# Kernel optimization log

Hardware: AMD Instinct MI355X
Metric: run time of the kernel (lower is better)

## Reference

```python
import jax, jax.numpy as jnp
import numpy as np

N_NODES = 100_000
N_EDGES = 1_600_000
IN_DIM = 500
HID = 128
OUT = 16
DEG = 3          # Chebyshev 'order' -> DEG+1 basis terms
N_KAN_USED = 2   # forward applies kan_layers[:num_layers-1] with num_layers=3


def spmm(edge_index, h):
    # torch.sparse.mm(A, h) with A = COO(edge_index, ones, (N, N)):
    # out[row] = sum over edges of h[col]
    return jax.ops.segment_sum(h[edge_index[1]], edge_index[0], num_segments=N_NODES)


def cheb_kan(h, coeffs):
    # ChebyKANLayer: t = tanh(h); basis T_k(t) = cos(k*arccos(t)) computed via
    # the (mathematically identical, numerically stable) recurrence.
    t = jnp.tanh(h)                                  # [N, HID]
    Ts = [jnp.ones_like(t), t]
    for _ in range(DEG - 1):
        Ts.append(2.0 * t * Ts[-1] - Ts[-2])
    basis = jnp.stack(Ts, axis=-1)                   # [N, HID, DEG+1]
    return jnp.einsum('nid,iod->no', basis, coeffs)  # [N, HID]


def setup_inputs() -> dict:
    key = jax.random.key(0)
    ks = jax.random.split(key, 6)
    x = jax.random.normal(ks[0], (N_NODES, IN_DIM), dtype=jnp.float32)
    edge_index = jax.random.randint(ks[1], (2, N_EDGES), 0, N_NODES)
    W_in = jax.random.normal(ks[2], (IN_DIM, HID), dtype=jnp.float32) / np.sqrt(IN_DIM)
    cheb_coeffs = jax.random.normal(ks[3], (N_KAN_USED, HID, HID, DEG + 1),
                                    dtype=jnp.float32) / (HID * (DEG + 1))
    W_out = jax.random.normal(ks[4], (HID, OUT), dtype=jnp.float32) / np.sqrt(HID)
    return {"x": x, "edge_index": edge_index, "W_in": W_in,
            "cheb_coeffs": cheb_coeffs, "W_out": W_out}


def reference(x, edge_index, W_in, cheb_coeffs, W_out):
    h = x @ W_in                      # linear_input (no bias)
    # dropout is identity at inference
    h = spmm(edge_index, h)           # sparse adjacency aggregation
    for l in range(N_KAN_USED):
        h = cheb_kan(h, cheb_coeffs[l])
        h = spmm(edge_index, h)
    logits = h @ W_out                # output_layer (no bias)
    return jax.nn.log_softmax(logits, axis=-1)
```

## Files before the change

### kernel.cpp

```cpp
#include <hip/hip_runtime.h>
#include <hip/hip_bf16.h>

#define N_NODES 100000
#define N_EDGES 1600000
#define IN_DIM  500
#define HID     128
#define KDIM    512
#define NB      782
#define BCAP    4096

typedef __attribute__((ext_vector_type(8))) short bf16x8;
typedef __attribute__((ext_vector_type(4))) float f32x4;

__device__ inline short f2bf(float x) {
    union { float f; unsigned u; } v; v.f = x;
    unsigned r = (v.u + 0x7FFFu + ((v.u >> 16) & 1u)) >> 16;
    return (short)r;
}
__device__ inline float bf_lo(unsigned u) { union { unsigned u; float f; } v; v.u = u << 16; return v.f; }
__device__ inline float bf_hi(unsigned u) { union { unsigned u; float f; } v; v.u = u & 0xFFFF0000u; return v.f; }
__device__ inline float bf2f(unsigned short s) { union { unsigned u; float f; } v; v.u = ((unsigned)s) << 16; return v.f; }


__global__ __launch_bounds__(256) void bin_kernel(const int* __restrict__ ei,
                                                  int* __restrict__ bcnt,
                                                  unsigned* __restrict__ buf) {
    int e = blockIdx.x * 256 + threadIdx.x;
    if (e < N_EDGES) {
        int r = ei[e];
        int c = ei[N_EDGES + e];
        int b = r >> 7;
        int p = atomicAdd(&bcnt[b * 16], 1);
        if (p < BCAP) buf[b * BCAP + p] = ((unsigned)(r & 127) << 17) | (unsigned)c;
    }
}

__global__ __launch_bounds__(1024) void bscan_kernel(const int* __restrict__ bcnt,
                                                     int* __restrict__ bbase) {
    __shared__ int buf[1024];
    const int tid = threadIdx.x;
    int v = (tid < NB) ? bcnt[tid * 16] : 0;
    buf[tid] = v;
    __syncthreads();
    for (int off = 1; off < 1024; off <<= 1) {
        int t = (tid >= off) ? buf[tid - off] : 0;
        __syncthreads();
        buf[tid] += t;
        __syncthreads();
    }
    if (tid < NB) bbase[tid] = buf[tid] - v;
}

__global__ __launch_bounds__(256) void place_kernel(const unsigned* __restrict__ buf,
                                                    const int* __restrict__ bcnt,
                                                    const int* __restrict__ bbase,
                                                    int* __restrict__ row_start,
                                                    int* __restrict__ col_sorted) {
    __shared__ int hist[128];
    __shared__ int scan[128];
    __shared__ int cur[128];
    const int b = blockIdx.x, tid = threadIdx.x;
    int cnt = bcnt[b * 16]; if (cnt > BCAP) cnt = BCAP;
    const int base = bbase[b];
    if (tid < 128) hist[tid] = 0;
    __syncthreads();
    for (int i = tid; i < cnt; i += 256)
        atomicAdd(&hist[buf[b * BCAP + i] >> 17], 1);
    __syncthreads();
    if (tid < 128) scan[tid] = hist[tid];
    __syncthreads();
    for (int off = 1; off < 128; off <<= 1) {
        int t = (tid < 128 && tid >= off) ? scan[tid - off] : 0;
        __syncthreads();
        if (tid < 128) scan[tid] += t;
        __syncthreads();
    }
    if (tid < 128) {
        int excl = scan[tid] - hist[tid] + base;
        cur[tid] = excl;
        int r = b * 128 + tid;
        if (r < N_NODES) row_start[r] = excl;
        if (r == N_NODES - 1) row_start[N_NODES] = excl + hist[tid];
    }
    __syncthreads();
    for (int i = tid; i < cnt; i += 256) {
        unsigned u = buf[b * BCAP + i];
        int rl = (int)(u >> 17);
        int c  = (int)(u & 0x1FFFFu);
        int pos = atomicAdd(&cur[rl], 1);
        col_sorted[pos] = c;
    }
}

__global__ __launch_bounds__(256) void repack_cheb(const float* __restrict__ cheb,
                                                   unsigned short* __restrict__ Bmat) {
    int idx = blockIdx.x * 256 + threadIdx.x;
    int o = idx >> 9;
    int k = idx & 511;
    int i = k >> 2;
    int d = k & 3;
    Bmat[idx] = (unsigned short)f2bf(cheb[i * 512 + o * 4 + d]);
}
__global__ __launch_bounds__(256) void repack_w(const float* __restrict__ W,
                                                unsigned short* __restrict__ Wmat) {
    int idx = blockIdx.x * 256 + threadIdx.x;
    int o = idx >> 9;
    int k = idx & 511;
    Wmat[idx] = (k < IN_DIM) ? (unsigned short)f2bf(W[k * HID + o]) : 0;
}
__global__ __launch_bounds__(256) void repack_c2w(const float* __restrict__ cheb,
                                                  const float* __restrict__ Wout,
                                                  unsigned short* __restrict__ C2W) {
    int idx = blockIdx.x * 256 + threadIdx.x;
    if (idx >= 16 * 512) return;
    int o16 = idx >> 9;
    int k   = idx & 511;
    const float* cb = cheb + 65536 + (k >> 2) * 512 + (k & 3);
    float s = 0.f;
#pragma unroll 4
    for (int o = 0; o < 128; o++) s += cb[o * 4] * Wout[o * 16 + o16];
    C2W[o16 * 512 + k] = (unsigned short)f2bf(s);
}

__global__ __launch_bounds__(256, 4) void gemm_xw(const float* __restrict__ x,
                                                  const unsigned short* __restrict__ Wmat,
                                                  unsigned short* __restrict__ out) {
    __shared__ __align__(16) short As[2][64][40];
    __shared__ __align__(16) short Bs[2][128][40];
    const int tid  = threadIdx.x;
    const int lane = tid & 63;
    const int wave = tid >> 6;
    const int quad = lane >> 4;
    const int l16  = lane & 15;
    const int n0   = blockIdx.x * 64;
    const int ar   = tid >> 2;
    const int ah   = tid & 3;
    const int br   = tid >> 1;
    const int bh   = tid & 1;

    int nA = n0 + ar; if (nA >= N_NODES) nA = N_NODES - 1;
    const float* __restrict__ xrow = x + (long)nA * IN_DIM;

    f32x4 acc[8];
#pragma unroll
    for (int nt = 0; nt < 8; nt++)
#pragma unroll
        for (int r = 0; r < 4; r++) acc[nt][r] = 0.f;

    auto loadA = [&](int kt, float (&v)[8]) {
        const int kb = kt * 32 + ah * 8;
        if (kb + 8 <= IN_DIM) {
            const float4* s4 = (const float4*)(xrow + kb);
            float4 a0 = s4[0], a1 = s4[1];
            v[0]=a0.x; v[1]=a0.y; v[2]=a0.z; v[3]=a0.w;
            v[4]=a1.x; v[5]=a1.y; v[6]=a1.z; v[7]=a1.w;
        } else {
#pragma unroll
            for (int q = 0; q < 8; q++) v[q] = (kb + q < IN_DIM) ? xrow[kb + q] : 0.f;
        }
    };
    auto loadB = [&](int kt, bf16x8 (&w)[2]) {
        w[0] = *(const bf16x8*)&Wmat[br * 512 + kt * 32 + bh * 16];
        w[1] = *(const bf16x8*)&Wmat[br * 512 + kt * 32 + bh * 16 + 8];
    };
    auto storeA = [&](int buf, const float (&v)[8]) {
        short t[8];
#pragma unroll
        for (int q = 0; q < 8; q++) t[q] = f2bf(v[q]);
        *(bf16x8*)&As[buf][ar][ah * 8] = *(bf16x8*)&t[0];
    };
    auto storeB = [&](int buf, const bf16x8 (&w)[2]) {
        *(bf16x8*)&Bs[buf][br][bh * 16]     = w[0];
        *(bf16x8*)&Bs[buf][br][bh * 16 + 8] = w[1];
    };
    auto mfmaTile = [&](int buf) {
        bf16x8 a = *(const bf16x8*)&As[buf][wave * 16 + l16][quad * 8];
#pragma unroll
        for (int nt = 0; nt < 8; nt++) {
            bf16x8 b = *(const bf16x8*)&Bs[buf][nt * 16 + l16][quad * 8];
            acc[nt] = __builtin_amdgcn_mfma_f32_16x16x32_bf16(a, b, acc[nt], 0, 0, 0);
        }
    };

    float  va[8], vb[8];
    bf16x8 wa[2], wb[2];
    loadA(0, va); loadB(0, wa);
    for (int kt = 0; kt < 16; kt += 2) {
        storeA(0, va); storeB(0, wa);
        loadA(kt + 1, vb); loadB(kt + 1, wb);
        __syncthreads();
        mfmaTile(0);
        storeA(1, vb); storeB(1, wb);
        if (kt + 2 < 16) { loadA(kt + 2, va); loadB(kt + 2, wa); }
        __syncthreads();
        mfmaTile(1);
    }

    {
        int mrow = n0 + wave * 16 + quad * 4;
#pragma unroll
        for (int r = 0; r < 4; r++) {
            int n = mrow + r;
            if (n < N_NODES) {
#pragma unroll
                for (int nt = 0; nt < 8; nt++)
                    out[(long)n * HID + nt * 16 + l16] = (unsigned short)f2bf(acc[nt][r]);
            }
        }
    }
}

__global__ __launch_bounds__(256, 4) void cheb_gemm(const unsigned short* __restrict__ h,
                                                    const unsigned short* __restrict__ Bmat,
                                                    unsigned short* __restrict__ out) {
    __shared__ __align__(16) short As[2][64][40];
    __shared__ __align__(16) short Bs[2][128][40];
    const int tid  = threadIdx.x;
    const int lane = tid & 63;
    const int wave = tid >> 6;
    const int quad = lane >> 4;
    const int l16  = lane & 15;
    const int n0   = blockIdx.x * 64;
    const int ar   = tid >> 2;
    const int sub  = tid & 3;
    const int br   = tid >> 1;
    const int bh   = tid & 1;

    int nA = n0 + ar; if (nA >= N_NODES) nA = N_NODES - 1;
    const unsigned short* __restrict__ hrow = h + (long)nA * HID;

    f32x4 acc[8];
#pragma unroll
    for (int nt = 0; nt < 8; nt++)
#pragma unroll
        for (int r = 0; r < 4; r++) acc[nt][r] = 0.f;

    auto loadA = [&](int kt, unsigned& v) {
        v = *(const unsigned*)(hrow + kt * 8 + sub * 2);
    };
    auto loadB = [&](int kt, bf16x8 (&w)[2]) {
        w[0] = *(const bf16x8*)&Bmat[br * 512 + kt * 32 + bh * 16];
        w[1] = *(const bf16x8*)&Bmat[br * 512 + kt * 32 + bh * 16 + 8];
    };
    auto storeA = [&](int buf, unsigned v) {
        float hx[2] = {bf_lo(v), bf_hi(v)};
        short t[8];
#pragma unroll
        for (int q = 0; q < 2; q++) {
            float xx = fminf(fmaxf(hx[q], -15.f), 15.f);
            float e  = __expf(2.f * xx);
            float tt = (e - 1.f) / (e + 1.f);
            float T2 = 2.f * tt * tt - 1.f;
            float T3 = 2.f * tt * T2 - tt;
            t[q * 4 + 0] = (short)0x3F80;
            t[q * 4 + 1] = f2bf(tt);
            t[q * 4 + 2] = f2bf(T2);
            t[q * 4 + 3] = f2bf(T3);
        }
        *(bf16x8*)&As[buf][ar][sub * 8] = *(bf16x8*)&t[0];
    };
    auto storeB = [&](int buf, const bf16x8 (&w)[2]) {
        *(bf16x8*)&Bs[buf][br][bh * 16]     = w[0];
        *(bf16x8*)&Bs[buf][br][bh * 16 + 8] = w[1];
    };
    auto mfmaTile = [&](int buf) {
        bf16x8 a = *(const bf16x8*)&As[buf][wave * 16 + l16][quad * 8];
#pragma unroll
        for (int nt = 0; nt < 8; nt++) {
            bf16x8 b = *(const bf16x8*)&Bs[buf][nt * 16 + l16][quad * 8];
            acc[nt] = __builtin_amdgcn_mfma_f32_16x16x32_bf16(a, b, acc[nt], 0, 0, 0);
        }
    };

    unsigned va, vb;
    bf16x8   wa[2], wb[2];
    loadA(0, va); loadB(0, wa);
    for (int kt = 0; kt < 16; kt += 2) {
        storeA(0, va); storeB(0, wa);
        loadA(kt + 1, vb); loadB(kt + 1, wb);
        __syncthreads();
        mfmaTile(0);
        storeA(1, vb); storeB(1, wb);
        if (kt + 2 < 16) { loadA(kt + 2, va); loadB(kt + 2, wa); }
        __syncthreads();
        mfmaTile(1);
    }

    {
        int mrow = n0 + wave * 16 + quad * 4;
#pragma unroll
        for (int r = 0; r < 4; r++) {
            int n = mrow + r;
            if (n < N_NODES) {
#pragma unroll
                for (int nt = 0; nt < 8; nt++)
                    out[(long)n * HID + nt * 16 + l16] = (unsigned short)f2bf(acc[nt][r]);
            }
        }
    }
}

__global__ __launch_bounds__(256, 4) void cheb16_gemm(const unsigned short* __restrict__ h,
                                                      const unsigned short* __restrict__ C2W,
                                                      float* __restrict__ z) {
    __shared__ __align__(16) short As[2][64][40];
    __shared__ __align__(16) short Bs16[16][520];
    const int tid  = threadIdx.x;
    const int lane = tid & 63;
    const int wave = tid >> 6;
    const int quad = lane >> 4;
    const int l16  = lane & 15;
    const int n0   = blockIdx.x * 64;
    const int ar   = tid >> 2;
    const int sub  = tid & 3;

    {
        int o16 = tid >> 4;
        int seg = tid & 15;
        *(bf16x8*)&Bs16[o16][seg * 32]      = *(const bf16x8*)&C2W[o16 * 512 + seg * 32];
        *(bf16x8*)&Bs16[o16][seg * 32 + 8]  = *(const bf16x8*)&C2W[o16 * 512 + seg * 32 + 8];
        *(bf16x8*)&Bs16[o16][seg * 32 + 16] = *(const bf16x8*)&C2W[o16 * 512 + seg * 32 + 16];
        *(bf16x8*)&Bs16[o16][seg * 32 + 24] = *(const bf16x8*)&C2W[o16 * 512 + seg * 32 + 24];
    }

    int nA = n0 + ar; if (nA >= N_NODES) nA = N_NODES - 1;
    const unsigned short* __restrict__ hrow = h + (long)nA * HID;

    f32x4 acc;
#pragma unroll
    for (int r = 0; r < 4; r++) acc[r] = 0.f;

    auto loadA = [&](int kt, unsigned& v) {
        v = *(const unsigned*)(hrow + kt * 8 + sub * 2);
    };
    auto storeA = [&](int buf, unsigned v) {
        float hx[2] = {bf_lo(v), bf_hi(v)};
        short t[8];
#pragma unroll
        for (int q = 0; q < 2; q++) {
            float xx = fminf(fmaxf(hx[q], -15.f), 15.f);
            float e  = __expf(2.f * xx);
            float tt = (e - 1.f) / (e + 1.f);
            float T2 = 2.f * tt * tt - 1.f;
            float T3 = 2.f * tt * T2 - tt;
            t[q * 4 + 0] = (short)0x3F80;
            t[q * 4 + 1] = f2bf(tt);
            t[q * 4 + 2] = f2bf(T2);
            t[q * 4 + 3] = f2bf(T3);
        }
        *(bf16x8*)&As[buf][ar][sub * 8] = *(bf16x8*)&t[0];
    };
    auto mfmaTile = [&](int buf, int kt) {
        bf16x8 a = *(const bf16x8*)&As[buf][wave * 16 + l16][quad * 8];
        bf16x8 b = *(const bf16x8*)&Bs16[l16][kt * 32 + quad * 8];
        acc = __builtin_amdgcn_mfma_f32_16x16x32_bf16(a, b, acc, 0, 0, 0);
    };

    unsigned va, vb;
    loadA(0, va);
    for (int kt = 0; kt < 16; kt += 2) {
        storeA(0, va);
        loadA(kt + 1, vb);
        __syncthreads();
        mfmaTile(0, kt);
        storeA(1, vb);
        if (kt + 2 < 16) loadA(kt + 2, va);
        __syncthreads();
        mfmaTile(1, kt + 1);
    }

    {
        int mrow = n0 + wave * 16 + quad * 4;
#pragma unroll
        for (int r = 0; r < 4; r++) {
            int n = mrow + r;
            if (n < N_NODES) z[n * 16 + l16] = acc[r];
        }
    }
}

__global__ __launch_bounds__(256) void spmm_gather(const int* __restrict__ row_start,
                                                   const int* __restrict__ col_sorted,
                                                   const unsigned short* __restrict__ h,
                                                   unsigned short* __restrict__ out) {
    const int wid  = (blockIdx.x * 256 + threadIdx.x) >> 6;
    const int lane = threadIdx.x & 63;
    const int sub  = lane >> 4;
    const int fl   = lane & 15;
    if (wid >= N_NODES) return;
    const int s = row_start[wid];
    const int e = row_start[wid + 1];
    const uint4* __restrict__ h4 = (const uint4*)h;

    float a[8], b[8];
#pragma unroll
    for (int q = 0; q < 8; q++) { a[q] = 0.f; b[q] = 0.f; }

    int j = s;
    for (; j + 8 <= e; j += 8) {
        int c0 = col_sorted[j + sub];
        int c1 = col_sorted[j + 4 + sub];
        uint4 u0 = h4[c0 * 16 + fl];
        uint4 u1 = h4[c1 * 16 + fl];
        a[0] += bf_lo(u0.x); a[1] += bf_hi(u0.x);
        a[2] += bf_lo(u0.y); a[3] += bf_hi(u0.y);
        a[4] += bf_lo(u0.z); a[5] += bf_hi(u0.z);
        a[6] += bf_lo(u0.w); a[7] += bf_hi(u0.w);
        b[0] += bf_lo(u1.x); b[1] += bf_hi(u1.x);
        b[2] += bf_lo(u1.y); b[3] += bf_hi(u1.y);
        b[4] += bf_lo(u1.z); b[5] += bf_hi(u1.z);
        b[6] += bf_lo(u1.w); b[7] += bf_hi(u1.w);
    }
    for (; j < e; j += 4) {
        int idx = j + sub;
        float m = (idx < e) ? 1.f : 0.f;
        int ci = (idx < e) ? idx : (e - 1);
        int c = col_sorted[ci];
        uint4 u = h4[c * 16 + fl];
        a[0] = fmaf(m, bf_lo(u.x), a[0]); a[1] = fmaf(m, bf_hi(u.x), a[1]);
        a[2] = fmaf(m, bf_lo(u.y), a[2]); a[3] = fmaf(m, bf_hi(u.y), a[3]);
        a[4] = fmaf(m, bf_lo(u.z), a[4]); a[5] = fmaf(m, bf_hi(u.z), a[5]);
        a[6] = fmaf(m, bf_lo(u.w), a[6]); a[7] = fmaf(m, bf_hi(u.w), a[7]);
    }
#pragma unroll
    for (int q = 0; q < 8; q++) a[q] += b[q];
#pragma unroll
    for (int q = 0; q < 8; q++) {
        a[q] += __shfl_xor(a[q], 16);
        a[q] += __shfl_xor(a[q], 32);
    }
    if (sub == 0) {
        unsigned w0 = (unsigned)(unsigned short)f2bf(a[0]) | ((unsigned)(unsigned short)f2bf(a[1]) << 16);
        unsigned w1 = (unsigned)(unsigned short)f2bf(a[2]) | ((unsigned)(unsigned short)f2bf(a[3]) << 16);
        unsigned w2 = (unsigned)(unsigned short)f2bf(a[4]) | ((unsigned)(unsigned short)f2bf(a[5]) << 16);
        unsigned w3 = (unsigned)(unsigned short)f2bf(a[6]) | ((unsigned)(unsigned short)f2bf(a[7]) << 16);
        uint4 pw; pw.x = w0; pw.y = w1; pw.z = w2; pw.w = w3;
        ((uint4*)out)[wid * 16 + fl] = pw;
    }
}

__global__ __launch_bounds__(256) void spmm_out(const int* __restrict__ row_start,
                                                const int* __restrict__ col_sorted,
                                                const float* __restrict__ z,
                                                float* __restrict__ out) {
    const int wid  = (blockIdx.x * 256 + threadIdx.x) >> 6;
    const int lane = threadIdx.x & 63;
    const int sub  = lane >> 4;
    const int fl   = lane & 15;
    if (wid >= N_NODES) return;
    const int s = row_start[wid];
    const int e = row_start[wid + 1];

    float a0 = 0.f, a1 = 0.f;
    int j = s;
    for (; j + 8 <= e; j += 8) {
        int c0 = col_sorted[j + sub];
        int c1 = col_sorted[j + 4 + sub];
        a0 += z[c0 * 16 + fl];
        a1 += z[c1 * 16 + fl];
    }
    for (; j < e; j += 4) {
        int idx = j + sub;
        float m = (idx < e) ? 1.f : 0.f;
        int ci = (idx < e) ? idx : (e - 1);
        a0 = fmaf(m, z[col_sorted[ci] * 16 + fl], a0);
    }
    float v = a0 + a1;
    v += __shfl_xor(v, 16);
    v += __shfl_xor(v, 32);
    float mx = v;
#pragma unroll
    for (int m = 8; m >= 1; m >>= 1) mx = fmaxf(mx, __shfl_xor(mx, m));
    float ex = expf(v - mx);
    float se = ex;
#pragma unroll
    for (int m = 8; m >= 1; m >>= 1) se += __shfl_xor(se, m);
    if (sub == 0) out[wid * 16 + fl] = v - mx - logf(se);
}


extern "C" void kernel_launch(void* const* d_in, const int* in_sizes, int n_in,
                              void* d_out, int out_size, void* d_ws, size_t ws_size,
                              hipStream_t stream) {
    const float* x     = (const float*)d_in[0];
    const int*   ei    = (const int*)d_in[1];
    const float* W_in  = (const float*)d_in[2];
    const float* cheb  = (const float*)d_in[3];
    const float* W_out = (const float*)d_in[4];
    float* out = (float*)d_out;

    char* p = (char*)d_ws;
    unsigned short* hA   = (unsigned short*)p; p += (size_t)N_NODES * HID * 2;
    unsigned short* hB   = (unsigned short*)p; p += (size_t)N_NODES * HID * 2;
    int*   col_sorted    = (int*)p;            p += (size_t)N_EDGES * 4;
    unsigned short* Bmat = (unsigned short*)p; p += (size_t)HID * KDIM * 2;
    unsigned short* Wmat = (unsigned short*)p; p += (size_t)HID * KDIM * 2;
    unsigned short* C2W  = (unsigned short*)p; p += (size_t)16 * KDIM * 2;
    float* zbuf          = (float*)p;          p += (size_t)N_NODES * 16 * 4;
    int*   row_start     = (int*)p;            p += (size_t)(N_NODES + 1) * 4;
    int*   bcnt          = (int*)p;            p += (size_t)NB * 16 * 4;
    int*   bbase         = (int*)p;            p += (size_t)NB * 4;

    unsigned* bbuf = (unsigned*)hA;

    const int nblk_gemm = (N_NODES + 63) / 64;
    const int nblk_edge = N_EDGES / 256;
    const int nblk_spmm = (N_NODES + 3) / 4;

    hipMemsetAsync(bcnt, 0, (size_t)NB * 16 * 4, stream);
    bin_kernel<<<nblk_edge, 256, 0, stream>>>(ei, bcnt, bbuf);
    bscan_kernel<<<1, 1024, 0, stream>>>(bcnt, bbase);
    place_kernel<<<NB, 256, 0, stream>>>(bbuf, bcnt, bbase, row_start, col_sorted);
    repack_cheb<<<HID * KDIM / 256, 256, 0, stream>>>(cheb, Bmat);
    repack_w<<<HID * KDIM / 256, 256, 0, stream>>>(W_in, Wmat);
    repack_c2w<<<16 * KDIM / 256, 256, 0, stream>>>(cheb, W_out, C2W);

    gemm_xw<<<nblk_gemm, 256, 0, stream>>>(x, Wmat, hA);
    spmm_gather<<<nblk_spmm, 256, 0, stream>>>(row_start, col_sorted, hA, hB);

    cheb_gemm<<<nblk_gemm, 256, 0, stream>>>(hB, Bmat, hA);
    spmm_gather<<<nblk_spmm, 256, 0, stream>>>(row_start, col_sorted, hA, hB);

    cheb16_gemm<<<nblk_gemm, 256, 0, stream>>>(hB, C2W, zbuf);
    spmm_out<<<nblk_spmm, 256, 0, stream>>>(row_start, col_sorted, zbuf, out);
}
```

Baseline: 653.4 us.

## Store GEMM outputs feature-sliced and run SpMM gather per 16-feature slice

The two GEMMs feeding the SpMM now write their outputs in a slice-major layout of 8 slices with 16 features each. The SpMM kernel launches 8x more blocks, each handling one 16-feature slice per node with 16 edges in flight per wave. With blockIdx.x & 7 choosing the slice, the 8 slices of the same nodes run at about the same time, and each gather pass touches a 3.2MB slice that fits in cache, so random neighbour reads should hit L2 or the last-level cache more often. The cost is narrower 8-byte loads per lane, 8x the row_start and col_sorted reads, and more shuffle-reduction steps.

```diff
diff --git a/kernel.cpp b/kernel.cpp
--- a/kernel.cpp
+++ b/kernel.cpp
@@ -204,7 +204,7 @@
             if (n < N_NODES) {
 #pragma unroll
                 for (int nt = 0; nt < 8; nt++)
-                    out[(long)n * HID + nt * 16 + l16] = (unsigned short)f2bf(acc[nt][r]);
+                    out[((long)nt * N_NODES + n) * 16 + l16] = (unsigned short)f2bf(acc[nt][r]);
             }
         }
     }
@@ -294,7 +294,7 @@
             if (n < N_NODES) {
 #pragma unroll
                 for (int nt = 0; nt < 8; nt++)
-                    out[(long)n * HID + nt * 16 + l16] = (unsigned short)f2bf(acc[nt][r]);
+                    out[((long)nt * N_NODES + n) * 16 + l16] = (unsigned short)f2bf(acc[nt][r]);
             }
         }
     }
@@ -379,63 +379,50 @@
     }
 }
 
-__global__ __launch_bounds__(256) void spmm_gather(const int* __restrict__ row_start,
+__global__ __launch_bounds__(256) void spmm_sliced(const int* __restrict__ row_start,
                                                    const int* __restrict__ col_sorted,
-                                                   const unsigned short* __restrict__ h,
+                                                   const unsigned short* __restrict__ h_sm,
                                                    unsigned short* __restrict__ out) {
-    const int wid  = (blockIdx.x * 256 + threadIdx.x) >> 6;
+    const int s    = blockIdx.x & 7;
+    const int wid  = (((blockIdx.x >> 3) * 256) + (int)threadIdx.x) >> 6;
     const int lane = threadIdx.x & 63;
-    const int sub  = lane >> 4;
-    const int fl   = lane & 15;
+    const int sub  = lane >> 2;
+    const int fl   = lane & 3;
     if (wid >= N_NODES) return;
-    const int s = row_start[wid];
-    const int e = row_start[wid + 1];
-    const uint4* __restrict__ h4 = (const uint4*)h;
-
-    float a[8], b[8];
-#pragma unroll
-    for (int q = 0; q < 8; q++) { a[q] = 0.f; b[q] = 0.f; }
-
-    int j = s;
-    for (; j + 8 <= e; j += 8) {
-        int c0 = col_sorted[j + sub];
-        int c1 = col_sorted[j + 4 + sub];
-        uint4 u0 = h4[c0 * 16 + fl];
-        uint4 u1 = h4[c1 * 16 + fl];
-        a[0] += bf_lo(u0.x); a[1] += bf_hi(u0.x);
-        a[2] += bf_lo(u0.y); a[3] += bf_hi(u0.y);
-        a[4] += bf_lo(u0.z); a[5] += bf_hi(u0.z);
-        a[6] += bf_lo(u0.w); a[7] += bf_hi(u0.w);
-        b[0] += bf_lo(u1.x); b[1] += bf_hi(u1.x);
-        b[2] += bf_lo(u1.y); b[3] += bf_hi(u1.y);
-        b[4] += bf_lo(u1.z); b[5] += bf_hi(u1.z);
-        b[6] += bf_lo(u1.w); b[7] += bf_hi(u1.w);
-    }
-    for (; j < e; j += 4) {
+    const int rs = row_start[wid];
+    const int re = row_start[wid + 1];
+    const uint2* __restrict__ hs = (const uint2*)h_sm + (long)s * N_NODES * 4;
+
+    float a0 = 0.f, a1 = 0.f, a2 = 0.f, a3 = 0.f;
+
+    int j = rs;
+    for (; j + 16 <= re; j += 16) {
+        int c = col_sorted[j + sub];
+        uint2 u = hs[c * 4 + fl];
+        a0 += bf_lo(u.x); a1 += bf_hi(u.x);
+        a2 += bf_lo(u.y); a3 += bf_hi(u.y);
+    }
+    if (j < re) {
         int idx = j + sub;
-        float m = (idx < e) ? 1.f : 0.f;
-        int ci = (idx < e) ? idx : (e - 1);
+        float m = (idx < re) ? 1.f : 0.f;
+        int ci  = (idx < re) ? idx : (re - 1);
         int c = col_sorted[ci];
-        uint4 u = h4[c * 16 + fl];
-        a[0] = fmaf(m, bf_lo(u.x), a[0]); a[1] = fmaf(m, bf_hi(u.x), a[1]);
-        a[2] = fmaf(m, bf_lo(u.y), a[2]); a[3] = fmaf(m, bf_hi(u.y), a[3]);
-        a[4] = fmaf(m, bf_lo(u.z), a[4]); a[5] = fmaf(m, bf_hi(u.z), a[5]);
-        a[6] = fmaf(m, bf_lo(u.w), a[6]); a[7] = fmaf(m, bf_hi(u.w), a[7]);
-    }
-#pragma unroll
-    for (int q = 0; q < 8; q++) a[q] += b[q];
-#pragma unroll
-    for (int q = 0; q < 8; q++) {
-        a[q] += __shfl_xor(a[q], 16);
-        a[q] += __shfl_xor(a[q], 32);
+        uint2 u = hs[c * 4 + fl];
+        a0 = fmaf(m, bf_lo(u.x), a0); a1 = fmaf(m, bf_hi(u.x), a1);
+        a2 = fmaf(m, bf_lo(u.y), a2); a3 = fmaf(m, bf_hi(u.y), a3);
+    }
+#pragma unroll
+    for (int mm = 4; mm <= 32; mm <<= 1) {
+        a0 += __shfl_xor(a0, mm);
+        a1 += __shfl_xor(a1, mm);
+        a2 += __shfl_xor(a2, mm);
+        a3 += __shfl_xor(a3, mm);
     }
     if (sub == 0) {
-        unsigned w0 = (unsigned)(unsigned short)f2bf(a[0]) | ((unsigned)(unsigned short)f2bf(a[1]) << 16);
-        unsigned w1 = (unsigned)(unsigned short)f2bf(a[2]) | ((unsigned)(unsigned short)f2bf(a[3]) << 16);
-        unsigned w2 = (unsigned)(unsigned short)f2bf(a[4]) | ((unsigned)(unsigned short)f2bf(a[5]) << 16);
-        unsigned w3 = (unsigned)(unsigned short)f2bf(a[6]) | ((unsigned)(unsigned short)f2bf(a[7]) << 16);
-        uint4 pw; pw.x = w0; pw.y = w1; pw.z = w2; pw.w = w3;
-        ((uint4*)out)[wid * 16 + fl] = pw;
+        uint2 pw;
+        pw.x = (unsigned)(unsigned short)f2bf(a0) | ((unsigned)(unsigned short)f2bf(a1) << 16);
+        pw.y = (unsigned)(unsigned short)f2bf(a2) | ((unsigned)(unsigned short)f2bf(a3) << 16);
+        *(uint2*)&out[(long)wid * HID + s * 16 + fl * 4] = pw;
     }
 }
 
@@ -503,9 +490,10 @@
 
     unsigned* bbuf = (unsigned*)hA;
 
-    const int nblk_gemm = (N_NODES + 63) / 64;
-    const int nblk_edge = N_EDGES / 256;
-    const int nblk_spmm = (N_NODES + 3) / 4;
+    const int nblk_gemm  = (N_NODES + 63) / 64;
+    const int nblk_edge  = N_EDGES / 256;
+    const int nblk_spmm  = (N_NODES + 3) / 4;
+    const int nblk_spmm8 = nblk_spmm * 8;
 
     hipMemsetAsync(bcnt, 0, (size_t)NB * 16 * 4, stream);
     bin_kernel<<<nblk_edge, 256, 0, stream>>>(ei, bcnt, bbuf);
@@ -516,10 +504,10 @@
     repack_c2w<<<16 * KDIM / 256, 256, 0, stream>>>(cheb, W_out, C2W);
 
     gemm_xw<<<nblk_gemm, 256, 0, stream>>>(x, Wmat, hA);
-    spmm_gather<<<nblk_spmm, 256, 0, stream>>>(row_start, col_sorted, hA, hB);
+    spmm_sliced<<<nblk_spmm8, 256, 0, stream>>>(row_start, col_sorted, hA, hB);
 
     cheb_gemm<<<nblk_gemm, 256, 0, stream>>>(hB, Bmat, hA);
-    spmm_gather<<<nblk_spmm, 256, 0, stream>>>(row_start, col_sorted, hA, hB);
+    spmm_sliced<<<nblk_spmm8, 256, 0, stream>>>(row_start, col_sorted, hA, hB);
 
     cheb16_gemm<<<nblk_gemm, 256, 0, stream>>>(hB, C2W, zbuf);
     spmm_out<<<nblk_spmm, 256, 0, stream>>>(row_start, col_sorted, zbuf, out);
```

New measurement: 909.8 us. 39.2% more time.

## Load A operands directly into MFMA registers and merge repack kernels

Applied to the files above, without the earlier changes.

The three GEMM kernels drop the shared-memory staging of the A tile. Each lane now loads its own row fragment from global memory, converts it or builds the Chebyshev basis in registers, and feeds it straight to the MFMA, which removes LDS writes, reads and some barrier work. The cheb kernels preload the whole 128-wide row into registers. The three weight-repack kernels are merged into one launch. In exchange the Chebyshev basis is now computed per wave rather than once per element cooperatively, register pressure rises, and the global load pattern for x changes.

```diff
diff --git a/kernel.cpp b/kernel.cpp
--- a/kernel.cpp
+++ b/kernel.cpp
@@ -19,7 +19,24 @@
 }
 __device__ inline float bf_lo(unsigned u) { union { unsigned u; float f; } v; v.u = u << 16; return v.f; }
 __device__ inline float bf_hi(unsigned u) { union { unsigned u; float f; } v; v.u = u & 0xFFFF0000u; return v.f; }
-__device__ inline float bf2f(unsigned short s) { union { unsigned u; float f; } v; v.u = ((unsigned)s) << 16; return v.f; }
+
+__device__ inline bf16x8 cheb_frag(unsigned v) {
+    float hx[2] = {bf_lo(v), bf_hi(v)};
+    short t[8];
+#pragma unroll
+    for (int q = 0; q < 2; q++) {
+        float xx = fminf(fmaxf(hx[q], -15.f), 15.f);
+        float e  = __expf(2.f * xx);
+        float tt = (e - 1.f) / (e + 1.f);
+        float T2 = 2.f * tt * tt - 1.f;
+        float T3 = 2.f * tt * T2 - tt;
+        t[q * 4 + 0] = (short)0x3F80;
+        t[q * 4 + 1] = f2bf(tt);
+        t[q * 4 + 2] = f2bf(T2);
+        t[q * 4 + 3] = f2bf(T3);
+    }
+    return *(bf16x8*)&t[0];
+}
 
 
 __global__ __launch_bounds__(256) void bin_kernel(const int* __restrict__ ei,
@@ -92,40 +109,40 @@
     }
 }
 
-__global__ __launch_bounds__(256) void repack_cheb(const float* __restrict__ cheb,
-                                                   unsigned short* __restrict__ Bmat) {
-    int idx = blockIdx.x * 256 + threadIdx.x;
-    int o = idx >> 9;
-    int k = idx & 511;
-    int i = k >> 2;
-    int d = k & 3;
-    Bmat[idx] = (unsigned short)f2bf(cheb[i * 512 + o * 4 + d]);
-}
-__global__ __launch_bounds__(256) void repack_w(const float* __restrict__ W,
-                                                unsigned short* __restrict__ Wmat) {
-    int idx = blockIdx.x * 256 + threadIdx.x;
-    int o = idx >> 9;
-    int k = idx & 511;
-    Wmat[idx] = (k < IN_DIM) ? (unsigned short)f2bf(W[k * HID + o]) : 0;
-}
-__global__ __launch_bounds__(256) void repack_c2w(const float* __restrict__ cheb,
+__global__ __launch_bounds__(256) void repack_all(const float* __restrict__ cheb,
+                                                  const float* __restrict__ W,
                                                   const float* __restrict__ Wout,
+                                                  unsigned short* __restrict__ Bmat,
+                                                  unsigned short* __restrict__ Wmat,
                                                   unsigned short* __restrict__ C2W) {
-    int idx = blockIdx.x * 256 + threadIdx.x;
-    if (idx >= 16 * 512) return;
-    int o16 = idx >> 9;
-    int k   = idx & 511;
-    const float* cb = cheb + 65536 + (k >> 2) * 512 + (k & 3);
-    float s = 0.f;
+    const int b = blockIdx.x;
+    if (b < 256) {
+        int idx = b * 256 + threadIdx.x;
+        int o = idx >> 9;
+        int k = idx & 511;
+        int i = k >> 2;
+        int d = k & 3;
+        Bmat[idx] = (unsigned short)f2bf(cheb[i * 512 + o * 4 + d]);
+    } else if (b < 512) {
+        int idx = (b - 256) * 256 + threadIdx.x;
+        int o = idx >> 9;
+        int k = idx & 511;
+        Wmat[idx] = (k < IN_DIM) ? (unsigned short)f2bf(W[k * HID + o]) : 0;
+    } else {
+        int idx = (b - 512) * 256 + threadIdx.x;
+        int o16 = idx >> 9;
+        int k   = idx & 511;
+        const float* cb = cheb + 65536 + (k >> 2) * 512 + (k & 3);
+        float s = 0.f;
 #pragma unroll 4
-    for (int o = 0; o < 128; o++) s += cb[o * 4] * Wout[o * 16 + o16];
-    C2W[o16 * 512 + k] = (unsigned short)f2bf(s);
+        for (int o = 0; o < 128; o++) s += cb[o * 4] * Wout[o * 16 + o16];
+        C2W[o16 * 512 + k] = (unsigned short)f2bf(s);
+    }
 }
 
 __global__ __launch_bounds__(256, 4) void gemm_xw(const float* __restrict__ x,
                                                   const unsigned short* __restrict__ Wmat,
                                                   unsigned short* __restrict__ out) {
-    __shared__ __align__(16) short As[2][64][40];
     __shared__ __align__(16) short Bs[2][128][40];
     const int tid  = threadIdx.x;
     const int lane = tid & 63;
@@ -133,13 +150,11 @@
     const int quad = lane >> 4;
     const int l16  = lane & 15;
     const int n0   = blockIdx.x * 64;
-    const int ar   = tid >> 2;
-    const int ah   = tid & 3;
     const int br   = tid >> 1;
     const int bh   = tid & 1;
 
-    int nA = n0 + ar; if (nA >= N_NODES) nA = N_NODES - 1;
-    const float* __restrict__ xrow = x + (long)nA * IN_DIM;
+    int row = n0 + wave * 16 + l16; if (row >= N_NODES) row = N_NODES - 1;
+    const float* __restrict__ xrow = x + (long)row * IN_DIM;
 
     f32x4 acc[8];
 #pragma unroll
@@ -148,7 +163,7 @@
         for (int r = 0; r < 4; r++) acc[nt][r] = 0.f;
 
     auto loadA = [&](int kt, float (&v)[8]) {
-        const int kb = kt * 32 + ah * 8;
+        const int kb = kt * 32 + quad * 8;
         if (kb + 8 <= IN_DIM) {
             const float4* s4 = (const float4*)(xrow + kb);
             float4 a0 = s4[0], a1 = s4[1];
@@ -163,18 +178,15 @@
         w[0] = *(const bf16x8*)&Wmat[br * 512 + kt * 32 + bh * 16];
         w[1] = *(const bf16x8*)&Wmat[br * 512 + kt * 32 + bh * 16 + 8];
     };
-    auto storeA = [&](int buf, const float (&v)[8]) {
-        short t[8];
-#pragma unroll
-        for (int q = 0; q < 8; q++) t[q] = f2bf(v[q]);
-        *(bf16x8*)&As[buf][ar][ah * 8] = *(bf16x8*)&t[0];
-    };
     auto storeB = [&](int buf, const bf16x8 (&w)[2]) {
         *(bf16x8*)&Bs[buf][br][bh * 16]     = w[0];
         *(bf16x8*)&Bs[buf][br][bh * 16 + 8] = w[1];
     };
-    auto mfmaTile = [&](int buf) {
-        bf16x8 a = *(const bf16x8*)&As[buf][wave * 16 + l16][quad * 8];
+    auto mfmaTile = [&](int buf, const float (&v)[8]) {
+        short t[8];
+#pragma unroll
+        for (int q = 0; q < 8; q++) t[q] = f2bf(v[q]);
+        bf16x8 a = *(bf16x8*)&t[0];
 #pragma unroll
         for (int nt = 0; nt < 8; nt++) {
             bf16x8 b = *(const bf16x8*)&Bs[buf][nt * 16 + l16][quad * 8];
@@ -186,14 +198,15 @@
     bf16x8 wa[2], wb[2];
     loadA(0, va); loadB(0, wa);
     for (int kt = 0; kt < 16; kt += 2) {
-        storeA(0, va); storeB(0, wa);
-        loadA(kt + 1, vb); loadB(kt + 1, wb);
-        __syncthreads();
-        mfmaTile(0);
-        storeA(1, vb); storeB(1, wb);
-        if (kt + 2 < 16) { loadA(kt + 2, va); loadB(kt + 2, wa); }
-        __syncthreads();
-        mfmaTile(1);
+        storeB(0, wa);
+        loadB(kt + 1, wb);
+        loadA(kt + 1, vb);
+        __syncthreads();
+        mfmaTile(0, va);
+        storeB(1, wb);
+        if (kt + 2 < 16) { loadB(kt + 2, wa); loadA(kt + 2, va); }
+        __syncthreads();
+        mfmaTile(1, vb);
     }
 
     {
@@ -213,7 +226,6 @@
 __global__ __launch_bounds__(256, 4) void cheb_gemm(const unsigned short* __restrict__ h,
                                                     const unsigned short* __restrict__ Bmat,
                                                     unsigned short* __restrict__ out) {
-    __shared__ __align__(16) short As[2][64][40];
     __shared__ __align__(16) short Bs[2][128][40];
     const int tid  = threadIdx.x;
     const int lane = tid & 63;
@@ -221,13 +233,16 @@
     const int quad = lane >> 4;
     const int l16  = lane & 15;
     const int n0   = blockIdx.x * 64;
-    const int ar   = tid >> 2;
-    const int sub  = tid & 3;
     const int br   = tid >> 1;
     const int bh   = tid & 1;
 
-    int nA = n0 + ar; if (nA >= N_NODES) nA = N_NODES - 1;
-    const unsigned short* __restrict__ hrow = h + (long)nA * HID;
+    int row = n0 + wave * 16 + l16; if (row >= N_NODES) row = N_NODES - 1;
+    const unsigned short* __restrict__ hrow = h + (long)row * HID;
+
+    unsigned hreg[16];
+#pragma unroll
+    for (int kt = 0; kt < 16; kt++)
+        hreg[kt] = *(const unsigned*)(hrow + kt * 8 + quad * 2);
 
     f32x4 acc[8];
 #pragma unroll
@@ -235,36 +250,16 @@
 #pragma unroll
         for (int r = 0; r < 4; r++) acc[nt][r] = 0.f;
 
-    auto loadA = [&](int kt, unsigned& v) {
-        v = *(const unsigned*)(hrow + kt * 8 + sub * 2);
-    };
     auto loadB = [&](int kt, bf16x8 (&w)[2]) {
         w[0] = *(const bf16x8*)&Bmat[br * 512 + kt * 32 + bh * 16];
         w[1] = *(const bf16x8*)&Bmat[br * 512 + kt * 32 + bh * 16 + 8];
     };
-    auto storeA = [&](int buf, unsigned v) {
-        float hx[2] = {bf_lo(v), bf_hi(v)};
-        short t[8];
-#pragma unroll
-        for (int q = 0; q < 2; q++) {
-            float xx = fminf(fmaxf(hx[q], -15.f), 15.f);
-            float e  = __expf(2.f * xx);
-            float tt = (e - 1.f) / (e + 1.f);
-            float T2 = 2.f * tt * tt - 1.f;
-            float T3 = 2.f * tt * T2 - tt;
-            t[q * 4 + 0] = (short)0x3F80;
-            t[q * 4 + 1] = f2bf(tt);
-            t[q * 4 + 2] = f2bf(T2);
-            t[q * 4 + 3] = f2bf(T3);
-        }
-        *(bf16x8*)&As[buf][ar][sub * 8] = *(bf16x8*)&t[0];
-    };
     auto storeB = [&](int buf, const bf16x8 (&w)[2]) {
         *(bf16x8*)&Bs[buf][br][bh * 16]     = w[0];
         *(bf16x8*)&Bs[buf][br][bh * 16 + 8] = w[1];
     };
-    auto mfmaTile = [&](int buf) {
-        bf16x8 a = *(const bf16x8*)&As[buf][wave * 16 + l16][quad * 8];
+    auto mfmaTile = [&](int buf, int kt) {
+        bf16x8 a = cheb_frag(hreg[kt]);
 #pragma unroll
         for (int nt = 0; nt < 8; nt++) {
             bf16x8 b = *(const bf16x8*)&Bs[buf][nt * 16 + l16][quad * 8];
@@ -272,18 +267,17 @@
         }
     };
 
-    unsigned va, vb;
-    bf16x8   wa[2], wb[2];
-    loadA(0, va); loadB(0, wa);
+    bf16x8 wa[2], wb[2];
+    loadB(0, wa);
     for (int kt = 0; kt < 16; kt += 2) {
-        storeA(0, va); storeB(0, wa);
-        loadA(kt + 1, vb); loadB(kt + 1, wb);
-        __syncthreads();
-        mfmaTile(0);
-        storeA(1, vb); storeB(1, wb);
-        if (kt + 2 < 16) { loadA(kt + 2, va); loadB(kt + 2, wa); }
-        __syncthreads();
-        mfmaTile(1);
+        storeB(0, wa);
+        loadB(kt + 1, wb);
+        __syncthreads();
+        mfmaTile(0, kt);
+        storeB(1, wb);
+        if (kt + 2 < 16) loadB(kt + 2, wa);
+        __syncthreads();
+        mfmaTile(1, kt + 1);
     }
 
     {
@@ -303,7 +297,6 @@
 __global__ __launch_bounds__(256, 4) void cheb16_gemm(const unsigned short* __restrict__ h,
                                                       const unsigned short* __restrict__ C2W,
                                                       float* __restrict__ z) {
-    __shared__ __align__(16) short As[2][64][40];
     __shared__ __align__(16) short Bs16[16][520];
     const int tid  = threadIdx.x;
     const int lane = tid & 63;
@@ -311,8 +304,6 @@
     const int quad = lane >> 4;
     const int l16  = lane & 15;
     const int n0   = blockIdx.x * 64;
-    const int ar   = tid >> 2;
-    const int sub  = tid & 3;
 
     {
         int o16 = tid >> 4;
@@ -323,50 +314,25 @@
         *(bf16x8*)&Bs16[o16][seg * 32 + 24] = *(const bf16x8*)&C2W[o16 * 512 + seg * 32 + 24];
     }
 
-    int nA = n0 + ar; if (nA >= N_NODES) nA = N_NODES - 1;
-    const unsigned short* __restrict__ hrow = h + (long)nA * HID;
+    int row = n0 + wave * 16 + l16; if (row >= N_NODES) row = N_NODES - 1;
+    const unsigned short* __restrict__ hrow = h + (long)row * HID;
+
+    unsigned hreg[16];
+#pragma unroll
+    for (int kt = 0; kt < 16; kt++)
+        hreg[kt] = *(const unsigned*)(hrow + kt * 8 + quad * 2);
 
     f32x4 acc;
 #pragma unroll
     for (int r = 0; r < 4; r++) acc[r] = 0.f;
 
-    auto loadA = [&](int kt, unsigned& v) {
-        v = *(const unsigned*)(hrow + kt * 8 + sub * 2);
-    };
-    auto storeA = [&](int buf, unsigned v) {
-        float hx[2] = {bf_lo(v), bf_hi(v)};
-        short t[8];
-#pragma unroll
-        for (int q = 0; q < 2; q++) {
-            float xx = fminf(fmaxf(hx[q], -15.f), 15.f);
-            float e  = __expf(2.f * xx);
-            float tt = (e - 1.f) / (e + 1.f);
-            float T2 = 2.f * tt * tt - 1.f;
-            float T3 = 2.f * tt * T2 - tt;
-            t[q * 4 + 0] = (short)0x3F80;
-            t[q * 4 + 1] = f2bf(tt);
-            t[q * 4 + 2] = f2bf(T2);
-            t[q * 4 + 3] = f2bf(T3);
-        }
-        *(bf16x8*)&As[buf][ar][sub * 8] = *(bf16x8*)&t[0];
-    };
-    auto mfmaTile = [&](int buf, int kt) {
-        bf16x8 a = *(const bf16x8*)&As[buf][wave * 16 + l16][quad * 8];
+    __syncthreads();
+
+#pragma unroll
+    for (int kt = 0; kt < 16; kt++) {
+        bf16x8 a = cheb_frag(hreg[kt]);
         bf16x8 b = *(const bf16x8*)&Bs16[l16][kt * 32 + quad * 8];
         acc = __builtin_amdgcn_mfma_f32_16x16x32_bf16(a, b, acc, 0, 0, 0);
-    };
-
-    unsigned va, vb;
-    loadA(0, va);
-    for (int kt = 0; kt < 16; kt += 2) {
-        storeA(0, va);
-        loadA(kt + 1, vb);
-        __syncthreads();
-        mfmaTile(0, kt);
-        storeA(1, vb);
-        if (kt + 2 < 16) loadA(kt + 2, va);
-        __syncthreads();
-        mfmaTile(1, kt + 1);
     }
 
     {
@@ -511,9 +477,7 @@
     bin_kernel<<<nblk_edge, 256, 0, stream>>>(ei, bcnt, bbuf);
     bscan_kernel<<<1, 1024, 0, stream>>>(bcnt, bbase);
     place_kernel<<<NB, 256, 0, stream>>>(bbuf, bcnt, bbase, row_start, col_sorted);
-    repack_cheb<<<HID * KDIM / 256, 256, 0, stream>>>(cheb, Bmat);
-    repack_w<<<HID * KDIM / 256, 256, 0, stream>>>(W_in, Wmat);
-    repack_c2w<<<16 * KDIM / 256, 256, 0, stream>>>(cheb, W_out, C2W);
+    repack_all<<<544, 256, 0, stream>>>(cheb, W_in, W_out, Bmat, Wmat, C2W);
 
     gemm_xw<<<nblk_gemm, 256, 0, stream>>>(x, Wmat, hA);
     spmm_gather<<<nblk_spmm, 256, 0, stream>>>(row_start, col_sorted, hA, hB);
```

After: 645.4 us. About the same (-1.2%).
